# Optimization experiments

Hardware: AMD Instinct MI355X
Metric: run time of the kernel (lower is better)

Reference implementation:

```python
import jax, jax.numpy as jnp
import numpy as np

N, E = 50000, 800000
IN, HID, OUT, H, REL, RD = 768, 256, 128, 8, 6, 64


def setup_inputs() -> dict:
    key = jax.random.key(0)
    ks = jax.random.split(key, 16)
    g = lambda i, shape, sc: jax.random.normal(ks[i], shape, jnp.float32) * sc
    return dict(
        x=g(0, (N, IN), 1.0),
        edge_index=jax.random.randint(ks[1], (2, E), 0, N),
        edge_type=jax.random.randint(ks[2], (E,), 0, REL),
        rel_emb=g(3, (REL, RD), 0.1),
        W1=g(4, (IN, HID), 0.03),
        att_src1=g(5, (H, HID // H), 0.1),
        att_dst1=g(6, (H, HID // H), 0.1),
        We1=g(7, (RD, HID), 0.1),
        att_e1=g(8, (H, HID // H), 0.1),
        b1=jnp.zeros((HID,), jnp.float32),
        g1=jnp.ones((HID,), jnp.float32),
        beta1=jnp.zeros((HID,), jnp.float32),
        W2=g(9, (HID, OUT), 0.06),
        att_src2=g(10, (1, OUT), 0.1),
        att_dst2=g(11, (1, OUT), 0.1),
        b2=jnp.zeros((OUT,), jnp.float32),
        g2=jnp.ones((OUT,), jnp.float32),
        beta2=jnp.zeros((OUT,), jnp.float32),
    )


def _gat(x, src, dst, W, a_s, a_d, bias, heads, ch, e_feat=None, We=None, a_e=None):
    # PyG GATConv (shared lin, concat=True, negative_slope=0.2, eval-mode dropout)
    n = x.shape[0]
    h = (x @ W).reshape(n, heads, ch)              # [N,H,C]
    al_s = (h * a_s).sum(-1)                       # [N,H]
    al_d = (h * a_d).sum(-1)
    alpha = al_s[src] + al_d[dst]                  # [Etot,H]
    if e_feat is not None:
        e = (e_feat @ We).reshape(-1, heads, ch)
        alpha = alpha + (e * a_e).sum(-1)
    alpha = jax.nn.leaky_relu(alpha, 0.2)
    mx = jax.ops.segment_max(alpha, dst, num_segments=n)   # segment softmax over dst
    ex = jnp.exp(alpha - mx[dst])
    den = jax.ops.segment_sum(ex, dst, num_segments=n)
    w = ex / (den[dst] + 1e-16)
    out = jax.ops.segment_sum(h[src] * w[:, :, None], dst, num_segments=n)
    return out.reshape(n, heads * ch) + bias


def _ln(x, g, b):
    m = x.mean(-1, keepdims=True)
    v = x.var(-1, keepdims=True)
    return (x - m) / jnp.sqrt(v + 1e-5) * g + b


def reference(x, edge_index, edge_type, rel_emb, W1, att_src1, att_dst1, We1, att_e1,
              b1, g1, beta1, W2, att_src2, att_dst2, b2, g2, beta2):
    n = x.shape[0]
    src0, dst0 = edge_index[0], edge_index[1]
    loop = jnp.arange(n)
    src = jnp.concatenate([src0, loop])
    dst = jnp.concatenate([dst0, loop])
    rel_feat = rel_emb[edge_type]                   # [E,RD]
    # self-loop edge_attr = mean of incoming edge_attr (fill_value='mean')
    cnt = jax.ops.segment_sum(jnp.ones((src0.shape[0],), jnp.float32), dst0, num_segments=n)
    self_attr = jax.ops.segment_sum(rel_feat, dst0, num_segments=n) / jnp.maximum(cnt, 1.0)[:, None]
    e_feat = jnp.concatenate([rel_feat, self_attr], 0)
    h = _gat(x, src, dst, W1, att_src1, att_dst1, b1, H, HID // H, e_feat, We1, att_e1)
    h = jax.nn.elu(_ln(h, g1, beta1))
    h = _gat(h, src, dst, W2, att_src2, att_dst2, b2, 1, OUT)
    return _ln(h, g2, beta2)
```

## Files before the change

kernel.cpp:

```cpp
#include <hip/hip_runtime.h>
#include <hip/hip_bf16.h>

#define IN_DIM 768
#define HID 256
#define OUT_DIM 128
#define NHEAD 8
#define NREL 6
#define RD 64

typedef unsigned short ushort_t;
typedef float f32x4 __attribute__((ext_vector_type(4)));
typedef __bf16 bf16x8 __attribute__((ext_vector_type(8)));
typedef unsigned short u16x8 __attribute__((ext_vector_type(8)));
typedef unsigned short u16x4 __attribute__((ext_vector_type(4)));
typedef unsigned short u16x2 __attribute__((ext_vector_type(2)));

typedef const __attribute__((address_space(1))) void* gptr_t;
typedef __attribute__((address_space(3))) void* lptr_t;

static __device__ __forceinline__ float leaky(float x) { return x > 0.f ? x : 0.2f * x; }

static __device__ __forceinline__ ushort_t f2bf(float f) {
    union { __hip_bfloat16 h; ushort_t u; } c;
    c.h = __float2bfloat16(f);
    return c.u;
}

static __device__ __forceinline__ float b2f(ushort_t u) {
    union { unsigned int i; float f; } c;
    c.i = ((unsigned int)u) << 16;
    return c.f;
}

__global__ void count_kernel(const int* __restrict__ dst0, int* __restrict__ deg, int E) {
    int e = blockIdx.x * blockDim.x + threadIdx.x;
    if (e >= E) return;
    atomicAdd(&deg[dst0[e]], 1);
}

__global__ void __launch_bounds__(256) scanA(const int* __restrict__ deg,
                                             int* __restrict__ bsum, int n) {
    __shared__ int sh[4];
    int b = blockIdx.x, t = threadIdx.x;
    int s = 0;
#pragma unroll
    for (int j = 0; j < 4; j++) {
        int idx = b * 1024 + t * 4 + j;
        if (idx < n) s += deg[idx];
    }
    for (int o = 32; o > 0; o >>= 1) s += __shfl_xor(s, o, 64);
    if ((t & 63) == 0) sh[t >> 6] = s;
    __syncthreads();
    if (t == 0) bsum[b] = sh[0] + sh[1] + sh[2] + sh[3];
}

__global__ void __launch_bounds__(256) scanB(const int* __restrict__ bsum,
                                             int* __restrict__ bbase,
                                             int* __restrict__ rowptr, int nb, int n) {
    __shared__ int sh[256];
    int t = threadIdx.x;
    int v = (t < nb) ? bsum[t] : 0;
    sh[t] = v;
    __syncthreads();
    for (int o = 1; o < 256; o <<= 1) {
        int add = (t >= o) ? sh[t - o] : 0;
        __syncthreads();
        sh[t] += add;
        __syncthreads();
    }
    if (t < nb) bbase[t] = sh[t] - v;
    if (t == 255) rowptr[n] = sh[255];
}

__global__ void __launch_bounds__(256) scanC(const int* __restrict__ deg,
                                             const int* __restrict__ bbase,
                                             int* __restrict__ rowptr, int n) {
    __shared__ int sh[256];
    int b = blockIdx.x, t = threadIdx.x;
    int base = b * 1024;
    int loc[4];
    int run = 0;
#pragma unroll
    for (int j = 0; j < 4; j++) {
        int idx = base + t * 4 + j;
        int d = (idx < n) ? deg[idx] : 0;
        loc[j] = run;
        run += d;
    }
    int tot = run;
    sh[t] = run;
    __syncthreads();
    for (int o = 1; o < 256; o <<= 1) {
        int add = (t >= o) ? sh[t - o] : 0;
        __syncthreads();
        sh[t] += add;
        __syncthreads();
    }
    int texcl = sh[t] - tot;
    int bb = bbase[b];
#pragma unroll
    for (int j = 0; j < 4; j++) {
        int idx = base + t * 4 + j;
        if (idx < n) rowptr[idx] = bb + texcl + loc[j];
    }
}

__global__ void scatter_kernel(const int* __restrict__ src0, const int* __restrict__ dst0,
                               const int* __restrict__ ety, const int* __restrict__ rowptr,
                               int* __restrict__ fill, int* __restrict__ src_pk, int E) {
    int e = blockIdx.x * blockDim.x + threadIdx.x;
    if (e >= E) return;
    int d = dst0[e];
    int pos = rowptr[d] + atomicAdd(&fill[d], 1);
    src_pk[pos] = src0[e] | (ety[e] << 24);
}

__global__ void rel_alpha_kernel(const float* __restrict__ rel_emb, const float* __restrict__ We1,
                                 const float* __restrict__ att_e1, float* __restrict__ rel_alpha) {
    int t = threadIdx.x;
    if (t >= NREL * NHEAD) return;
    int r = t / NHEAD, h = t % NHEAD;
    float acc = 0.f;
    for (int c = 0; c < HID / NHEAD; c++) {
        float v = 0.f;
        for (int k = 0; k < RD; k++) v += rel_emb[r * RD + k] * We1[k * HID + h * 32 + c];
        acc += v * att_e1[h * 32 + c];
    }
    rel_alpha[r * NHEAD + h] = acc;
}

__global__ void prep_weights(const float* __restrict__ W1, const float* __restrict__ W2,
                             ushort_t* __restrict__ W1t, ushort_t* __restrict__ W2t) {
    int i = blockIdx.x * 256 + threadIdx.x;
    if (i < IN_DIM * HID) {
        int k = i / HID, n = i % HID;
        W1t[n * IN_DIM + k] = f2bf(W1[i]);
    } else {
        int j = i - IN_DIM * HID;
        if (j < HID * OUT_DIM) {
            int k = j / OUT_DIM, n = j % OUT_DIM;
            W2t[n * HID + k] = f2bf(W2[j]);
        }
    }
}

__global__ void __launch_bounds__(256) gemm_f32a(const float* __restrict__ Af,
                                                 const ushort_t* __restrict__ Bt,
                                                 ushort_t* __restrict__ C,
                                                 int K, int Nout, int NBlk,
                                                 const float* __restrict__ att_s,
                                                 const float* __restrict__ att_d,
                                                 float* __restrict__ als,
                                                 float* __restrict__ ald, int N) {
    __shared__ float sAf[128 * 64];
    __shared__ ushort_t sB[128 * 64];
    int T = gridDim.x;
    int p = blockIdx.x;
    int q8 = T >> 3, rr8 = T & 7, xc = p & 7, jj0 = p >> 3;
    int l = (xc < rr8 ? xc * (q8 + 1) : rr8 * (q8 + 1) + (xc - rr8) * q8) + jj0;
    int m0 = (l / NBlk) * 128;
    int n0 = (l % NBlk) * 128;
    int t = threadIdx.x;
    int w = t >> 6, ln = t & 63;
    int wm = (w >> 1) * 64, wn = (w & 1) * 64;

    const float* agp[8];
#pragma unroll
    for (int i = 0; i < 8; i++) {
        int rl = w * 32 + i * 4 + (ln >> 4);
        int rg = min(m0 + rl, N - 1);
        int cc = (ln & 15) ^ (rl & 15);
        agp[i] = Af + (size_t)rg * K + (cc << 2);
    }
    const ushort_t* bgp[4];
#pragma unroll
    for (int i = 0; i < 4; i++) {
        int rl = w * 32 + i * 8 + (ln >> 3);
        int cc = (ln & 7) ^ (ln >> 3);
        bgp[i] = Bt + (size_t)(n0 + rl) * K + (cc << 3);
    }

    f32x4 acc[4][4] = {};

    for (int k0 = 0; k0 < K; k0 += 64) {
#pragma unroll
        for (int i = 0; i < 8; i++)
            __builtin_amdgcn_global_load_lds((gptr_t)(const void*)(agp[i] + k0),
                                             (lptr_t)(void*)(&sAf[(w * 32 + i * 4) * 64]),
                                             16, 0, 0);
#pragma unroll
        for (int i = 0; i < 4; i++)
            __builtin_amdgcn_global_load_lds((gptr_t)(const void*)(bgp[i] + k0),
                                             (lptr_t)(void*)(&sB[(w * 32 + i * 8) * 64]),
                                             16, 0, 0);
        __syncthreads();
#pragma unroll
        for (int ks = 0; ks < 2; ks++) {
            bf16x8 af[4], bfr[4];
#pragma unroll
            for (int m = 0; m < 4; m++) {
                int r = wm + m * 16 + (ln & 15);
                int key = ln & 15;
                int c0 = ks * 8 + (ln >> 4) * 2;
                const f32x4* rowp = reinterpret_cast<const f32x4*>(&sAf[r * 64]);
                f32x4 lo = rowp[c0 ^ key];
                f32x4 hi = rowp[(c0 + 1) ^ key];
                union { u16x8 u; bf16x8 b; } cv;
                cv.u[0] = f2bf(lo[0]); cv.u[1] = f2bf(lo[1]);
                cv.u[2] = f2bf(lo[2]); cv.u[3] = f2bf(lo[3]);
                cv.u[4] = f2bf(hi[0]); cv.u[5] = f2bf(hi[1]);
                cv.u[6] = f2bf(hi[2]); cv.u[7] = f2bf(hi[3]);
                af[m] = cv.b;
            }
#pragma unroll
            for (int n = 0; n < 4; n++) {
                int r = wn + n * 16 + (ln & 15);
                int key = ln & 7;
                int cB = ks * 4 + (ln >> 4);
                bfr[n] = *reinterpret_cast<const bf16x8*>(&sB[r * 64 + ((cB ^ key) << 3)]);
            }
#pragma unroll
            for (int m = 0; m < 4; m++)
#pragma unroll
                for (int n = 0; n < 4; n++)
                    acc[m][n] = __builtin_amdgcn_mfma_f32_16x16x32_bf16(af[m], bfr[n], acc[m][n], 0, 0, 0);
        }
        __syncthreads();
    }

    int cc = ln & 15, qq = ln >> 4;
#pragma unroll
    for (int m = 0; m < 4; m++) {
#pragma unroll
        for (int rr = 0; rr < 4; rr++) {
            int row = m0 + wm + m * 16 + qq * 4 + rr;
#pragma unroll
            for (int n = 0; n < 4; n++)
                C[(size_t)row * Nout + n0 + wn + n * 16 + cc] = f2bf(acc[m][n][rr]);
        }
    }

    float as_[4], ad_[4];
#pragma unroll
    for (int n = 0; n < 4; n++) {
        int col = n0 + wn + n * 16 + cc;
        as_[n] = att_s[col];
        ad_[n] = att_d[col];
    }
    int hbase = (n0 + wn) >> 5;
#pragma unroll
    for (int m = 0; m < 4; m++) {
#pragma unroll
        for (int rr = 0; rr < 4; rr++) {
            int row = m0 + wm + m * 16 + qq * 4 + rr;
            float ps0 = acc[m][0][rr] * as_[0] + acc[m][1][rr] * as_[1];
            float ps1 = acc[m][2][rr] * as_[2] + acc[m][3][rr] * as_[3];
            float pd0 = acc[m][0][rr] * ad_[0] + acc[m][1][rr] * ad_[1];
            float pd1 = acc[m][2][rr] * ad_[2] + acc[m][3][rr] * ad_[3];
#pragma unroll
            for (int o = 1; o < 16; o <<= 1) {
                ps0 += __shfl_xor(ps0, o, 64);
                ps1 += __shfl_xor(ps1, o, 64);
                pd0 += __shfl_xor(pd0, o, 64);
                pd1 += __shfl_xor(pd1, o, 64);
            }
            if (cc == 0 && row < N) {
                als[row * NHEAD + hbase] = ps0;
                als[row * NHEAD + hbase + 1] = ps1;
                ald[row * NHEAD + hbase] = pd0;
                ald[row * NHEAD + hbase + 1] = pd1;
            }
        }
    }
}

__global__ void __launch_bounds__(256) gemm_lds2(const ushort_t* __restrict__ A,
                                                 const ushort_t* __restrict__ Bt,
                                                 ushort_t* __restrict__ C,
                                                 int K, int Nout, int NBlk,
                                                 const float* __restrict__ att_s,
                                                 const float* __restrict__ att_d,
                                                 float* __restrict__ als,
                                                 float* __restrict__ ald, int N) {
    __shared__ ushort_t sA[2][128 * 32];
    __shared__ ushort_t sB[2][128 * 32];
    int T = gridDim.x;
    int p = blockIdx.x;
    int q8 = T >> 3, rr8 = T & 7, xc = p & 7, j = p >> 3;
    int l = (xc < rr8 ? xc * (q8 + 1) : rr8 * (q8 + 1) + (xc - rr8) * q8) + j;
    int m0 = (l / NBlk) * 128;
    int n0 = (l % NBlk) * 128;
    int t = threadIdx.x;
    int w = t >> 6, ln = t & 63;
    int wm = (w >> 1) * 64, wn = (w & 1) * 64;

    const ushort_t* ag = A + (size_t)(m0 + w * 32 + (ln >> 2)) * K + (ln & 3) * 8;
    const ushort_t* bg = Bt + (size_t)(n0 + w * 32 + (ln >> 2)) * K + (ln & 3) * 8;

    f32x4 acc[4][4] = {};

    auto stage = [&](int buf, int k0) {
#pragma unroll
        for (int i = 0; i < 2; i++) {
            __builtin_amdgcn_global_load_lds(
                (gptr_t)(const void*)(ag + (size_t)i * 16 * K + k0),
                (lptr_t)(void*)(&sA[buf][(w * 32 + i * 16) * 32]), 16, 0, 0);
            __builtin_amdgcn_global_load_lds(
                (gptr_t)(const void*)(bg + (size_t)i * 16 * K + k0),
                (lptr_t)(void*)(&sB[buf][(w * 32 + i * 16) * 32]), 16, 0, 0);
        }
    };

    int nt = K >> 5;
    stage(0, 0);
    __syncthreads();
    int cur = 0;
    for (int tt = 0; tt < nt; tt++) {
        if (tt + 1 < nt) stage(cur ^ 1, (tt + 1) << 5);
        bf16x8 af[4], bfr[4];
#pragma unroll
        for (int m = 0; m < 4; m++)
            af[m] = *reinterpret_cast<const bf16x8*>(
                &sA[cur][(wm + m * 16 + (ln & 15)) * 32 + (ln >> 4) * 8]);
#pragma unroll
        for (int n = 0; n < 4; n++)
            bfr[n] = *reinterpret_cast<const bf16x8*>(
                &sB[cur][(wn + n * 16 + (ln & 15)) * 32 + (ln >> 4) * 8]);
#pragma unroll
        for (int m = 0; m < 4; m++)
#pragma unroll
            for (int n = 0; n < 4; n++)
                acc[m][n] = __builtin_amdgcn_mfma_f32_16x16x32_bf16(af[m], bfr[n], acc[m][n], 0, 0, 0);
        __syncthreads();
        cur ^= 1;
    }

    int cc = ln & 15, qq = ln >> 4;
#pragma unroll
    for (int m = 0; m < 4; m++) {
#pragma unroll
        for (int rr = 0; rr < 4; rr++) {
            int row = m0 + wm + m * 16 + qq * 4 + rr;
#pragma unroll
            for (int n = 0; n < 4; n++)
                C[(size_t)row * Nout + n0 + wn + n * 16 + cc] = f2bf(acc[m][n][rr]);
        }
    }

    float as_[4], ad_[4];
#pragma unroll
    for (int n = 0; n < 4; n++) {
        int col = n0 + wn + n * 16 + cc;
        as_[n] = att_s[col];
        ad_[n] = att_d[col];
    }
    __shared__ float sh_s[2][128];
    __shared__ float sh_d[2][128];
#pragma unroll
    for (int m = 0; m < 4; m++) {
#pragma unroll
        for (int rr = 0; rr < 4; rr++) {
            int rib = wm + m * 16 + qq * 4 + rr;
            float ps = acc[m][0][rr] * as_[0] + acc[m][1][rr] * as_[1] +
                       acc[m][2][rr] * as_[2] + acc[m][3][rr] * as_[3];
            float pd = acc[m][0][rr] * ad_[0] + acc[m][1][rr] * ad_[1] +
                       acc[m][2][rr] * ad_[2] + acc[m][3][rr] * ad_[3];
#pragma unroll
            for (int o = 1; o < 16; o <<= 1) {
                ps += __shfl_xor(ps, o, 64);
                pd += __shfl_xor(pd, o, 64);
            }
            if (cc == 0) {
                sh_s[wn >> 6][rib] = ps;
                sh_d[wn >> 6][rib] = pd;
            }
        }
    }
    __syncthreads();
    if (t < 128) {
        int row = m0 + t;
        if (row < N) {
            als[row] = sh_s[0][t] + sh_s[1][t];
            ald[row] = sh_d[0][t] + sh_d[1][t];
        }
    }
}

__global__ void __launch_bounds__(256) node_agg1(
    const ushort_t* __restrict__ h1b, const float* __restrict__ als, const float* __restrict__ ald,
    const float* __restrict__ rel_alpha, const int* __restrict__ rowptr,
    const int* __restrict__ src_pk,
    const float* __restrict__ b1, const float* __restrict__ g1, const float* __restrict__ beta1,
    ushort_t* __restrict__ out, int N) {
    __shared__ float sh_rel[NREL * NHEAD];
    if (threadIdx.x < NREL * NHEAD) sh_rel[threadIdx.x] = rel_alpha[threadIdx.x];
    __syncthreads();
    int l = threadIdx.x & 63;
    int i = blockIdx.x * 4 + (threadIdx.x >> 6);
    if (i >= N) return;
    int h = l & 7;
    int e8 = l >> 3;
    float als_i = als[i * NHEAD + h];
    float ald_h = ald[i * NHEAD + h];
    float c0, c1, c2, c3;
    {
        u16x4 v = *reinterpret_cast<const u16x4*>(h1b + (size_t)i * HID + 4 * l);
        c0 = b2f(v[0]); c1 = b2f(v[1]); c2 = b2f(v[2]); c3 = b2f(v[3]);
    }
    int base = rowptr[i];
    int deg = rowptr[i + 1] - base;
    const char* hb = reinterpret_cast<const char*>(h1b);
    float acc0 = 0.f, acc1 = 0.f, acc2 = 0.f, acc3 = 0.f;
    float csum = 0.f, rs = 0.f;
    for (int cs = 0; cs < deg; cs += 8) {
        int c = min(8, deg - cs);
        float w = 0.f, ra = 0.f;
        unsigned offv = 0;
        if (e8 < c) {
            int pk = src_pk[base + cs + e8];
            int sv = pk & 0xFFFFFF;
            int tv = (unsigned)pk >> 24;
            ra = sh_rel[tv * NHEAD + h];
            w = __expf(fminf(leaky(als[sv * NHEAD + h] + ald_h + ra), 40.f));
            offv = (unsigned)sv * (HID * 2);
        }
        csum += w;
        rs += ra;
        if (c == 8) {
            float wt[8];
            unsigned of[8];
            u16x4 v[8];
#pragma unroll
            for (int e = 0; e < 8; e++) {
                wt[e] = __shfl(w, e * 8 + e8, 64);
                of[e] = (unsigned)__shfl((int)offv, e * 8, 64);
            }
#pragma unroll
            for (int e = 0; e < 8; e++)
                v[e] = *reinterpret_cast<const u16x4*>(hb + of[e] + 8 * l);
#pragma unroll
            for (int e = 0; e < 8; e++) {
                acc0 += wt[e] * b2f(v[e][0]);
                acc1 += wt[e] * b2f(v[e][1]);
                acc2 += wt[e] * b2f(v[e][2]);
                acc3 += wt[e] * b2f(v[e][3]);
            }
        } else {
            for (int e = 0; e < c; e++) {
                float wt = __shfl(w, e * 8 + e8, 64);
                unsigned of = (unsigned)__shfl((int)offv, e * 8, 64);
                u16x4 v = *reinterpret_cast<const u16x4*>(hb + of + 8 * l);
                acc0 += wt * b2f(v[0]); acc1 += wt * b2f(v[1]);
                acc2 += wt * b2f(v[2]); acc3 += wt * b2f(v[3]);
            }
        }
    }
    for (int o = 8; o < 64; o <<= 1) {
        csum += __shfl_xor(csum, o, 64);
        rs += __shfl_xor(rs, o, 64);
    }
    float selfa = rs / fmaxf((float)deg, 1.0f);
    float wself = __expf(fminf(leaky(als_i + ald_h + selfa), 40.f));
    float stot = csum + wself;
    float s_g = __shfl(stot, e8, 64);
    float w_g = __shfl(wself, e8, 64);
    acc0 += w_g * c0; acc1 += w_g * c1; acc2 += w_g * c2; acc3 += w_g * c3;
    float inv = 1.0f / (s_g + 1e-16f);
    float4 bb = *reinterpret_cast<const float4*>(b1 + 4 * l);
    float y0 = acc0 * inv + bb.x, y1 = acc1 * inv + bb.y;
    float y2 = acc2 * inv + bb.z, y3 = acc3 * inv + bb.w;
    float su = y0 + y1 + y2 + y3;
    float sq = y0 * y0 + y1 * y1 + y2 * y2 + y3 * y3;
    for (int o = 1; o < 64; o <<= 1) {
        su += __shfl_xor(su, o, 64);
        sq += __shfl_xor(sq, o, 64);
    }
    float mean = su * (1.f / 256.f);
    float var = sq * (1.f / 256.f) - mean * mean;
    float rstd = rsqrtf(var + 1e-5f);
    float4 gg = *reinterpret_cast<const float4*>(g1 + 4 * l);
    float4 be = *reinterpret_cast<const float4*>(beta1 + 4 * l);
    float z0 = (y0 - mean) * rstd * gg.x + be.x;
    float z1 = (y1 - mean) * rstd * gg.y + be.y;
    float z2 = (y2 - mean) * rstd * gg.z + be.z;
    float z3 = (y3 - mean) * rstd * gg.w + be.w;
    u16x4 ov;
    ov[0] = f2bf(z0 > 0.f ? z0 : __expf(z0) - 1.f);
    ov[1] = f2bf(z1 > 0.f ? z1 : __expf(z1) - 1.f);
    ov[2] = f2bf(z2 > 0.f ? z2 : __expf(z2) - 1.f);
    ov[3] = f2bf(z3 > 0.f ? z3 : __expf(z3) - 1.f);
    *reinterpret_cast<u16x4*>(out + (size_t)i * HID + 4 * l) = ov;
}

__global__ void __launch_bounds__(256) node_agg2(const ushort_t* __restrict__ h2b,
                                                 const float* __restrict__ als,
                                                 const float* __restrict__ ald,
                                                 const int* __restrict__ rowptr,
                                                 const int* __restrict__ src_pk,
                                                 const float* __restrict__ b2,
                                                 const float* __restrict__ g2,
                                                 const float* __restrict__ beta2,
                                                 float* __restrict__ out, int N) {
    int l = threadIdx.x & 63;
    int i = blockIdx.x * 4 + (threadIdx.x >> 6);
    if (i >= N) return;
    float aldi = ald[i];
    float alsi = als[i];
    float c0, c1;
    {
        u16x2 v = *reinterpret_cast<const u16x2*>(h2b + (size_t)i * OUT_DIM + 2 * l);
        c0 = b2f(v[0]); c1 = b2f(v[1]);
    }
    int base = rowptr[i];
    int deg = rowptr[i + 1] - base;
    const char* hb = reinterpret_cast<const char*>(h2b);
    float acc0 = 0.f, acc1 = 0.f;
    float csum = 0.f;
    for (int cs = 0; cs < deg; cs += 64) {
        int c = min(64, deg - cs);
        float w = 0.f;
        unsigned offv = 0;
        if (l < c) {
            int sv = src_pk[base + cs + l] & 0xFFFFFF;
            w = __expf(fminf(leaky(als[sv] + aldi), 40.f));
            offv = (unsigned)sv * (OUT_DIM * 2);
        }
        csum += w;
        int e = 0;
        for (; e + 8 <= c; e += 8) {
            float wt[8];
            unsigned of[8];
            u16x2 v[8];
#pragma unroll
            for (int jj = 0; jj < 8; jj++) {
                wt[jj] = __shfl(w, e + jj, 64);
                of[jj] = (unsigned)__shfl((int)offv, e + jj, 64);
            }
#pragma unroll
            for (int jj = 0; jj < 8; jj++)
                v[jj] = *reinterpret_cast<const u16x2*>(hb + of[jj] + 4 * l);
#pragma unroll
            for (int jj = 0; jj < 8; jj++) {
                acc0 += wt[jj] * b2f(v[jj][0]);
                acc1 += wt[jj] * b2f(v[jj][1]);
            }
        }
        for (; e < c; e++) {
            float wt = __shfl(w, e, 64);
            unsigned of = (unsigned)__shfl((int)offv, e, 64);
            u16x2 v = *reinterpret_cast<const u16x2*>(hb + of + 4 * l);
            acc0 += wt * b2f(v[0]); acc1 += wt * b2f(v[1]);
        }
    }
    for (int o = 1; o < 64; o <<= 1) csum += __shfl_xor(csum, o, 64);
    float wself = __expf(fminf(leaky(alsi + aldi), 40.f));
    float s = csum + wself;
    acc0 += wself * c0; acc1 += wself * c1;
    float inv = 1.0f / (s + 1e-16f);
    float2 bb = *reinterpret_cast<const float2*>(b2 + 2 * l);
    float y0 = acc0 * inv + bb.x, y1 = acc1 * inv + bb.y;
    float su = y0 + y1, sq = y0 * y0 + y1 * y1;
    for (int o = 1; o < 64; o <<= 1) {
        su += __shfl_xor(su, o, 64);
        sq += __shfl_xor(sq, o, 64);
    }
    float mean = su * (1.f / 128.f);
    float var = sq * (1.f / 128.f) - mean * mean;
    float rstd = rsqrtf(var + 1e-5f);
    float2 gg = *reinterpret_cast<const float2*>(g2 + 2 * l);
    float2 be = *reinterpret_cast<const float2*>(beta2 + 2 * l);
    float2 ov;
    ov.x = (y0 - mean) * rstd * gg.x + be.x;
    ov.y = (y1 - mean) * rstd * gg.y + be.y;
    *reinterpret_cast<float2*>(out + (size_t)i * OUT_DIM + 2 * l) = ov;
}

extern "C" void kernel_launch(void* const* d_in, const int* in_sizes, int n_in,
                              void* d_out, int out_size, void* d_ws, size_t ws_size,
                              hipStream_t stream) {
    const float* x = (const float*)d_in[0];
    const int* ei = (const int*)d_in[1];
    const int* ety = (const int*)d_in[2];
    const float* rel_emb = (const float*)d_in[3];
    const float* W1 = (const float*)d_in[4];
    const float* att_s1 = (const float*)d_in[5];
    const float* att_d1 = (const float*)d_in[6];
    const float* We1 = (const float*)d_in[7];
    const float* att_e1 = (const float*)d_in[8];
    const float* b1 = (const float*)d_in[9];
    const float* g1 = (const float*)d_in[10];
    const float* beta1 = (const float*)d_in[11];
    const float* W2 = (const float*)d_in[12];
    const float* att_s2 = (const float*)d_in[13];
    const float* att_d2 = (const float*)d_in[14];
    const float* b2 = (const float*)d_in[15];
    const float* g2 = (const float*)d_in[16];
    const float* beta2 = (const float*)d_in[17];

    int N = in_sizes[0] / IN_DIM;
    int E = in_sizes[1] / 2;
    int Mpad = ((N + 127) / 128) * 128;
    const int* src0 = ei;
    const int* dst0 = ei + E;

    char* ws = (char*)d_ws;
    size_t off = 0;
    auto alloc = [&](size_t bytes) -> void* {
        off = (off + 255) & ~(size_t)255;
        void* p = ws + off;
        off += bytes;
        return p;
    };
    int* deg = (int*)alloc((size_t)N * 4);
    int* fill = (int*)alloc((size_t)N * 4);
    int* rowptr = (int*)alloc((size_t)(N + 1) * 4);
    int* src_pk = (int*)alloc((size_t)E * 4);
    int nb = (N + 1023) >> 10;
    int* bsum = (int*)alloc((size_t)nb * 4);
    int* bbase = (int*)alloc((size_t)nb * 4);
    float* rel_alpha = (float*)alloc(NREL * NHEAD * 4);
    float* als1 = (float*)alloc((size_t)N * NHEAD * 4);
    float* ald1 = (float*)alloc((size_t)N * NHEAD * 4);
    float* al2s = (float*)alloc((size_t)N * 4);
    float* al2d = (float*)alloc((size_t)N * 4);
    ushort_t* W1t = (ushort_t*)alloc((size_t)HID * IN_DIM * 2);
    ushort_t* W2t = (ushort_t*)alloc((size_t)OUT_DIM * HID * 2);
    ushort_t* h1b = (ushort_t*)alloc((size_t)Mpad * HID * 2);
    ushort_t* h1pb = (ushort_t*)alloc((size_t)Mpad * HID * 2);
    ushort_t* h2b = h1b;

    hipMemsetAsync(deg, 0, (size_t)N * 4, stream);
    hipMemsetAsync(fill, 0, (size_t)N * 4, stream);

    int eb = (E + 255) / 256;
    count_kernel<<<eb, 256, 0, stream>>>(dst0, deg, E);
    scanA<<<nb, 256, 0, stream>>>(deg, bsum, N);
    scanB<<<1, 256, 0, stream>>>(bsum, bbase, rowptr, nb, N);
    scanC<<<nb, 256, 0, stream>>>(deg, bbase, rowptr, N);
    scatter_kernel<<<eb, 256, 0, stream>>>(src0, dst0, ety, rowptr, fill, src_pk, E);
    rel_alpha_kernel<<<1, 64, 0, stream>>>(rel_emb, We1, att_e1, rel_alpha);
    prep_weights<<<(IN_DIM * HID + HID * OUT_DIM + 255) / 256, 256, 0, stream>>>(W1, W2, W1t, W2t);

    int NB1 = HID / 128;
    int T1 = (Mpad / 128) * NB1;
    gemm_f32a<<<T1, 256, 0, stream>>>(x, W1t, h1b, IN_DIM, HID, NB1,
                                      att_s1, att_d1, als1, ald1, N);
    hipMemsetAsync(h1pb + (size_t)N * HID, 0, (size_t)(Mpad - N) * HID * 2, stream);
    node_agg1<<<(N + 3) / 4, 256, 0, stream>>>(h1b, als1, ald1, rel_alpha, rowptr, src_pk,
                                               b1, g1, beta1, h1pb, N);

    int NB2 = OUT_DIM / 128;
    int T2 = (Mpad / 128) * NB2;
    gemm_lds2<<<T2, 256, 0, stream>>>(h1pb, W2t, h2b, HID, OUT_DIM, NB2,
                                      att_s2, att_d2, al2s, al2d, N);
    node_agg2<<<(N + 3) / 4, 256, 0, stream>>>(h2b, al2s, al2d, rowptr, src_pk, b2, g2, beta2,
                                               (float*)d_out, N);
}
```

Measured before the change: 345.3 us.

## Double-buffer GEMM LDS tiles with explicit vmcnt waits and XOR swizzles

The fp32-A GEMM moves from a single-buffered 64-wide K tile to double-buffered 32-wide K tiles, so the next tile's global-to-LDS loads overlap MFMA work on the current one. Both GEMMs swap __syncthreads for explicit s_waitcnt vmcnt counts plus raw s_barrier, so only the older buffer's loads are waited on. The bf16 GEMM also gains an XOR swizzle on its LDS layout to cut bank conflicts. The hand-set vmcnt values must match the number of outstanding loads exactly, or reads may race with writes.

```diff
diff --git a/kernel.cpp b/kernel.cpp
--- a/kernel.cpp
+++ b/kernel.cpp
@@ -152,8 +152,8 @@
                                                  const float* __restrict__ att_d,
                                                  float* __restrict__ als,
                                                  float* __restrict__ ald, int N) {
-    __shared__ float sAf[128 * 64];
-    __shared__ ushort_t sB[128 * 64];
+    __shared__ float sAf[2][128 * 32];
+    __shared__ ushort_t sB[2][128 * 32];
     int T = gridDim.x;
     int p = blockIdx.x;
     int q8 = T >> 3, rr8 = T & 7, xc = p & 7, jj0 = p >> 3;
@@ -164,47 +164,59 @@
     int w = t >> 6, ln = t & 63;
     int wm = (w >> 1) * 64, wn = (w & 1) * 64;
 
-    const float* agp[8];
-#pragma unroll
-    for (int i = 0; i < 8; i++) {
-        int rl = w * 32 + i * 4 + (ln >> 4);
-        int rg = min(m0 + rl, N - 1);
-        int cc = (ln & 15) ^ (rl & 15);
-        agp[i] = Af + (size_t)rg * K + (cc << 2);
-    }
-    const ushort_t* bgp[4];
+    const float* agp[4];
 #pragma unroll
     for (int i = 0; i < 4; i++) {
         int rl = w * 32 + i * 8 + (ln >> 3);
+        int rg = min(m0 + rl, N - 1);
         int cc = (ln & 7) ^ (ln >> 3);
+        agp[i] = Af + (size_t)rg * K + (cc << 2);
+    }
+    const ushort_t* bgp[2];
+#pragma unroll
+    for (int i = 0; i < 2; i++) {
+        int rl = w * 32 + i * 16 + (ln >> 2);
+        int cc = (ln & 3) ^ ((ln >> 3) & 3);
         bgp[i] = Bt + (size_t)(n0 + rl) * K + (cc << 3);
     }
 
     f32x4 acc[4][4] = {};
 
-    for (int k0 = 0; k0 < K; k0 += 64) {
-#pragma unroll
-        for (int i = 0; i < 8; i++)
+    auto stage = [&](int buf, int k0) {
+#pragma unroll
+        for (int i = 0; i < 4; i++)
             __builtin_amdgcn_global_load_lds((gptr_t)(const void*)(agp[i] + k0),
-                                             (lptr_t)(void*)(&sAf[(w * 32 + i * 4) * 64]),
+                                             (lptr_t)(void*)(&sAf[buf][(w * 32 + i * 8) * 32]),
                                              16, 0, 0);
 #pragma unroll
-        for (int i = 0; i < 4; i++)
+        for (int i = 0; i < 2; i++)
             __builtin_amdgcn_global_load_lds((gptr_t)(const void*)(bgp[i] + k0),
-                                             (lptr_t)(void*)(&sB[(w * 32 + i * 8) * 64]),
+                                             (lptr_t)(void*)(&sB[buf][(w * 32 + i * 16) * 32]),
                                              16, 0, 0);
-        __syncthreads();
-#pragma unroll
-        for (int ks = 0; ks < 2; ks++) {
+    };
+
+    int nt = K >> 5;
+    int cur = 0;
+    stage(0, 0);
+    for (int tt = 0; tt < nt; tt++) {
+        if (tt + 1 < nt) {
+            stage(cur ^ 1, (tt + 1) << 5);
+            asm volatile("s_waitcnt vmcnt(6)" ::: "memory");
+        } else {
+            asm volatile("s_waitcnt vmcnt(0)" ::: "memory");
+        }
+        __builtin_amdgcn_sched_barrier(0);
+        __builtin_amdgcn_s_barrier();
+        {
             bf16x8 af[4], bfr[4];
 #pragma unroll
             for (int m = 0; m < 4; m++) {
                 int r = wm + m * 16 + (ln & 15);
-                int key = ln & 15;
-                int c0 = ks * 8 + (ln >> 4) * 2;
-                const f32x4* rowp = reinterpret_cast<const f32x4*>(&sAf[r * 64]);
-                f32x4 lo = rowp[c0 ^ key];
-                f32x4 hi = rowp[(c0 + 1) ^ key];
+                int key = r & 7;
+                int q = ln >> 4;
+                const f32x4* rowp = reinterpret_cast<const f32x4*>(&sAf[cur][r * 32]);
+                f32x4 lo = rowp[(2 * q) ^ key];
+                f32x4 hi = rowp[(2 * q + 1) ^ key];
                 union { u16x8 u; bf16x8 b; } cv;
                 cv.u[0] = f2bf(lo[0]); cv.u[1] = f2bf(lo[1]);
                 cv.u[2] = f2bf(lo[2]); cv.u[3] = f2bf(lo[3]);
@@ -215,9 +227,9 @@
 #pragma unroll
             for (int n = 0; n < 4; n++) {
                 int r = wn + n * 16 + (ln & 15);
-                int key = ln & 7;
-                int cB = ks * 4 + (ln >> 4);
-                bfr[n] = *reinterpret_cast<const bf16x8*>(&sB[r * 64 + ((cB ^ key) << 3)]);
+                int key = (r >> 1) & 3;
+                int q = ln >> 4;
+                bfr[n] = *reinterpret_cast<const bf16x8*>(&sB[cur][r * 32 + ((q ^ key) << 3)]);
             }
 #pragma unroll
             for (int m = 0; m < 4; m++)
@@ -225,7 +237,8 @@
                 for (int n = 0; n < 4; n++)
                     acc[m][n] = __builtin_amdgcn_mfma_f32_16x16x32_bf16(af[m], bfr[n], acc[m][n], 0, 0, 0);
         }
-        __syncthreads();
+        __builtin_amdgcn_s_barrier();
+        cur ^= 1;
     }
 
     int cc = ln & 15, qq = ln >> 4;
@@ -294,44 +307,64 @@
     int w = t >> 6, ln = t & 63;
     int wm = (w >> 1) * 64, wn = (w & 1) * 64;
 
-    const ushort_t* ag = A + (size_t)(m0 + w * 32 + (ln >> 2)) * K + (ln & 3) * 8;
-    const ushort_t* bg = Bt + (size_t)(n0 + w * 32 + (ln >> 2)) * K + (ln & 3) * 8;
+    const ushort_t* agp[2];
+    const ushort_t* bgp[2];
+#pragma unroll
+    for (int i = 0; i < 2; i++) {
+        int rl = w * 32 + i * 16 + (ln >> 2);
+        int cc = (ln & 3) ^ ((ln >> 3) & 3);
+        agp[i] = A + (size_t)(m0 + rl) * K + (cc << 3);
+        bgp[i] = Bt + (size_t)(n0 + rl) * K + (cc << 3);
+    }
 
     f32x4 acc[4][4] = {};
 
     auto stage = [&](int buf, int k0) {
 #pragma unroll
         for (int i = 0; i < 2; i++) {
-            __builtin_amdgcn_global_load_lds(
-                (gptr_t)(const void*)(ag + (size_t)i * 16 * K + k0),
-                (lptr_t)(void*)(&sA[buf][(w * 32 + i * 16) * 32]), 16, 0, 0);
-            __builtin_amdgcn_global_load_lds(
-                (gptr_t)(const void*)(bg + (size_t)i * 16 * K + k0),
-                (lptr_t)(void*)(&sB[buf][(w * 32 + i * 16) * 32]), 16, 0, 0);
+            __builtin_amdgcn_global_load_lds((gptr_t)(const void*)(agp[i] + k0),
+                                             (lptr_t)(void*)(&sA[buf][(w * 32 + i * 16) * 32]),
+                                             16, 0, 0);
+            __builtin_amdgcn_global_load_lds((gptr_t)(const void*)(bgp[i] + k0),
+                                             (lptr_t)(void*)(&sB[buf][(w * 32 + i * 16) * 32]),
+                                             16, 0, 0);
         }
     };
 
     int nt = K >> 5;
+    int cur = 0;
     stage(0, 0);
-    __syncthreads();
-    int cur = 0;
     for (int tt = 0; tt < nt; tt++) {
-        if (tt + 1 < nt) stage(cur ^ 1, (tt + 1) << 5);
-        bf16x8 af[4], bfr[4];
-#pragma unroll
-        for (int m = 0; m < 4; m++)
-            af[m] = *reinterpret_cast<const bf16x8*>(
-                &sA[cur][(wm + m * 16 + (ln & 15)) * 32 + (ln >> 4) * 8]);
-#pragma unroll
-        for (int n = 0; n < 4; n++)
-            bfr[n] = *reinterpret_cast<const bf16x8*>(
-                &sB[cur][(wn + n * 16 + (ln & 15)) * 32 + (ln >> 4) * 8]);
-#pragma unroll
-        for (int m = 0; m < 4; m++)
-#pragma unroll
-            for (int n = 0; n < 4; n++)
-                acc[m][n] = __builtin_amdgcn_mfma_f32_16x16x32_bf16(af[m], bfr[n], acc[m][n], 0, 0, 0);
-        __syncthreads();
+        if (tt + 1 < nt) {
+            stage(cur ^ 1, (tt + 1) << 5);
+            asm volatile("s_waitcnt vmcnt(4)" ::: "memory");
+        } else {
+            asm volatile("s_waitcnt vmcnt(0)" ::: "memory");
+        }
+        __builtin_amdgcn_sched_barrier(0);
+        __builtin_amdgcn_s_barrier();
+        {
+            bf16x8 af[4], bfr[4];
+            int q = ln >> 4;
+#pragma unroll
+            for (int m = 0; m < 4; m++) {
+                int r = wm + m * 16 + (ln & 15);
+                int key = (r >> 1) & 3;
+                af[m] = *reinterpret_cast<const bf16x8*>(&sA[cur][r * 32 + ((q ^ key) << 3)]);
+            }
+#pragma unroll
+            for (int n = 0; n < 4; n++) {
+                int r = wn + n * 16 + (ln & 15);
+                int key = (r >> 1) & 3;
+                bfr[n] = *reinterpret_cast<const bf16x8*>(&sB[cur][r * 32 + ((q ^ key) << 3)]);
+            }
+#pragma unroll
+            for (int m = 0; m < 4; m++)
+#pragma unroll
+                for (int n = 0; n < 4; n++)
+                    acc[m][n] = __builtin_amdgcn_mfma_f32_16x16x32_bf16(af[m], bfr[n], acc[m][n], 0, 0, 0);
+        }
+        __builtin_amdgcn_s_barrier();
         cur ^= 1;
     }
 
```

Measured after the change: 356.6 us. +3.3%, slower.
